# Optimization experiments

Measured on AMD Instinct MI355X. Metric: run time of the kernel, lower is better.

The kernel has to match this reference:

```python
import jax, jax.numpy as jnp
import numpy as np

K = 5  # kernel_size in context_loss
R = K // 2
COS_EPS = 1e-8  # F.cosine_similarity default eps


def _context_loss(er_input, seg_label, gt_boundary_seg):
    # er_input: [B,C,H,W] float; seg_label: [B,2,H,W] one-hot int; gt_boundary_seg: [B,H,W] int
    B, C, H, W = er_input.shape
    f32 = er_input.dtype

    gb = jnp.where(gt_boundary_seg == 255, 0, gt_boundary_seg)          # [B,H,W]
    slc = jnp.where(seg_label == 255, 0, seg_label)                     # [B,2,H,W]
    # gt_b = gt_boundary (broadcast over class dim) * seg_label; only channel 1 is used
    gt_b1 = gb * slc[:, 1]                                              # [B,H,W]
    boundary = gt_b1 > 0

    # interior margin so that all 5x5 neighbor shifts stay in-bounds
    iy = jnp.arange(H)
    ix = jnp.arange(W)
    interior = ((iy >= R) & (iy <= H - 1 - R))[:, None] & ((ix >= R) & (ix <= W - 1 - R))[None, :]
    sel = boundary & interior                                           # selected boundary pixels
    cnt = jnp.sum(sel, axis=(1, 2)).astype(f32)                         # [B]
    valid = jnp.sum(boundary, axis=(1, 2)) >= 1                         # batch participates (cal_mask.sum()>=1)

    nf = jnp.sqrt(jnp.sum(er_input * er_input, axis=1))                 # [B,H,W] feature norms
    seg_f = seg_label.astype(f32)

    shifts = [(ki - R, kj - R) for ki in range(K) for kj in range(K) if not (ki == R and kj == R)]
    loss_b = jnp.zeros((B,), f32)
    for dy, dx in shifts:
        # rolled[y,x] == orig[y+dy, x+dx]; wraparound is harmless since sel is interior-only
        fs = jnp.roll(er_input, (-dy, -dx), axis=(2, 3))
        ns = jnp.roll(nf, (-dy, -dx), axis=(1, 2))
        dot = jnp.sum(er_input * fs, axis=1)                            # [B,H,W]
        cos = dot / (jnp.maximum(nf, COS_EPS) * jnp.maximum(ns, COS_EPS))
        lab = jnp.sum(seg_f * jnp.roll(seg_f, (-dy, -dx), axis=(2, 3)), axis=1)
        se = jnp.where(sel, (cos - lab) ** 2, 0.0)
        loss_b = loss_b + jnp.sum(se, axis=(1, 2)) / jnp.maximum(cnt, 1.0)  # per-batch MSE for this shift
    loss_b = loss_b / len(shifts)

    n_valid = jnp.sum(valid.astype(f32))
    total = jnp.sum(jnp.where(valid, loss_b, 0.0)) / jnp.maximum(n_valid, 1.0)
    return jnp.where(jnp.isnan(total), jnp.zeros((), f32), total)


def setup_inputs() -> dict:
    key = jax.random.key(0)
    k1, k2, k3 = jax.random.split(key, 3)
    B, C, H, W = 4, 128, 384, 384
    er_input = jax.random.normal(k1, (B, C, H, W), dtype=jnp.float32)
    cls = jax.random.randint(k2, (B, H, W), 0, 2)
    seg_label = jnp.transpose(jax.nn.one_hot(cls, 2, dtype=jnp.int32), (0, 3, 1, 2))  # [B,2,H,W] one-hot
    gt_boundary_seg = jax.random.randint(k3, (B, H, W), 0, 2).astype(jnp.int32)
    return {"er_input": er_input, "seg_label": seg_label, "gt_boundary_seg": gt_boundary_seg}


def reference(er_input, seg_label, gt_boundary_seg):
    return _context_loss(er_input, seg_label, gt_boundary_seg)
```

## Files before the change

kernel.cpp:

```cpp
#include <hip/hip_runtime.h>
#include <math.h>

#define BB 4
#define CCH 128
#define HH 384
#define WW 384

constexpr int TILE_X = 64;
constexpr int TILE_Y = 16;
constexpr int CC = 4;
constexpr int NCHUNK = CCH / CC;
constexpr int ROWS = TILE_Y + 2;
constexpr int STR  = 72;
constexpr int GR   = 18;
constexpr int NVEC = CC * ROWS * GR;
constexpr int NLD  = 6;
constexpr int NSTR = 76;
#define EPSQ 1e-8f


__global__ __launch_bounds__(256, 3)
void ctx_main(const float* __restrict__ er, const int* __restrict__ seg,
              const int* __restrict__ gt, float* __restrict__ Ssum,
              int* __restrict__ cntArr, int* __restrict__ bndArr)
{
    __shared__ __align__(16) float buf0[CC * ROWS * STR];
    __shared__ __align__(16) float buf1[CC * ROWS * STR];
    __shared__ __align__(16) float normArr[ROWS * NSTR];

    const int tx  = threadIdx.x;
    const int ty  = threadIdx.y;
    const int tid = ty * 16 + tx;
    const int x0  = blockIdx.x * TILE_X;
    const int y0  = blockIdx.y * TILE_Y;
    const int b   = blockIdx.z;

    int srcOff[NLD];
    #pragma unroll
    for (int j = 0; j < NLD; ++j) {
        int id = tid + 256 * j; if (id > NVEC - 1) id = NVEC - 1;
        int c   = id / (ROWS * GR);
        int rem = id - c * (ROWS * GR);
        int r   = rem / GR;
        int g   = rem - r * GR;
        int gy  = y0 + r; if (gy > HH - 1) gy = HH - 1;
        int gx  = x0 - 4 + 4 * g;
        gx = min(max(gx, 0), WW - 4);
        srcOff[j] = (c * HH + gy) * WW + gx;
    }

    int hr = -1, hc = 0;
    if (tid < 136) { hr = TILE_Y + tid / 68; hc = 2 + tid % 68; }
    else if (tid < 200) {
        int t = tid - 136;
        hr = t >> 2;
        int j = t & 3;
        hc = (j < 2) ? (2 + j) : (66 + j);
    }

    float acc[12][4];
    #pragma unroll
    for (int s = 0; s < 12; ++s)
        #pragma unroll
        for (int i = 0; i < 4; ++i) acc[s][i] = 0.f;
    float nrm[4] = {0.f, 0.f, 0.f, 0.f};
    float haloN = 0.f;

    const float* erB = er + (size_t)b * CCH * HH * WW;

    auto issue = [&](int chunk, float* dst) {
        const float* erC = erB + (size_t)chunk * CC * HH * WW;
        #pragma unroll
        for (int j = 0; j < NLD; ++j) {
            int id = tid + 256 * j;
            if (j < NLD - 1 || id < NVEC) {
                __builtin_amdgcn_global_load_lds(
                    (const __attribute__((address_space(1))) void*)(erC + srcOff[j]),
                    (__attribute__((address_space(3))) void*)(dst + 4 * id),
                    16, 0, 0);
            }
        }
    };

    issue(0, buf0);

    for (int chunk = 0; chunk < NCHUNK; ++chunk) {
        float* cur = (chunk & 1) ? buf1 : buf0;
        __syncthreads();
        if (chunk + 1 < NCHUNK) issue(chunk + 1, (chunk & 1) ? buf0 : buf1);

        #pragma unroll
        for (int c = 0; c < CC; ++c) {
            const float* rp = &cur[(c * ROWS + ty) * STR + 4 * tx];
            float L0[12], L1[12], L2[12];
            #pragma unroll
            for (int jj = 0; jj < 3; ++jj) {
                *(float4*)&L0[4 * jj] = *(const float4*)(rp + 4 * jj);
                *(float4*)&L1[4 * jj] = *(const float4*)(rp + STR + 4 * jj);
                *(float4*)&L2[4 * jj] = *(const float4*)(rp + 2 * STR + 4 * jj);
            }
            #pragma unroll
            for (int i = 0; i < 4; ++i) {
                float f = L0[4 + i];
                nrm[i]    = fmaf(f, f,         nrm[i]);
                acc[0][i] = fmaf(f, L0[5 + i], acc[0][i]);
                acc[1][i] = fmaf(f, L0[6 + i], acc[1][i]);
                #pragma unroll
                for (int d = 0; d < 5; ++d) {
                    acc[2 + d][i] = fmaf(f, L1[2 + i + d], acc[2 + d][i]);
                    acc[7 + d][i] = fmaf(f, L2[2 + i + d], acc[7 + d][i]);
                }
            }
        }
        if (hr >= 0) {
            #pragma unroll
            for (int c = 0; c < CC; ++c) {
                float v = cur[(c * ROWS + hr) * STR + hc];
                haloN = fmaf(v, v, haloN);
            }
        }
    }

    __syncthreads();

    int* pkT = (int*)buf0;
    for (int it = tid; it < ROWS * STR; it += 256) {
        int r = it / STR, a = it - r * STR;
        int gy = y0 + r;
        int gx = x0 - 4 + a;
        int pk = 0;
        if (gy < HH && gx >= 0 && gx < WW) {
            int g   = gt[((size_t)b * HH + gy) * WW + gx];
            int gb  = (g == 255) ? 0 : g;
            int s0v = seg[(((size_t)b * 2 + 0) * HH + gy) * WW + gx];
            int s1v = seg[(((size_t)b * 2 + 1) * HH + gy) * WW + gx];
            int s1c = (s1v == 255) ? 0 : s1v;
            bool bnd   = (gb * s1c) > 0;
            bool inter = (gy >= 2 && gy <= HH - 3 && gx >= 2 && gx <= WW - 3);
            pk = (bnd ? 1 : 0) | ((bnd && inter) ? 2 : 0)
               | ((s0v & 255) << 8) | ((s1v & 255) << 16);
        }
        pkT[it] = pk;
    }
    #pragma unroll
    for (int i = 0; i < 4; ++i)
        normArr[ty * NSTR + 4 * tx + 4 + i] = sqrtf(nrm[i]);
    if (hr >= 0) normArr[hr * NSTR + hc] = sqrtf(haloN);
    __syncthreads();

    const float* nr = &normArr[ty * NSTR + 4 * tx];
    const int*   pr = &pkT[ty * STR + 4 * tx];
    float n0[12], n1[12], n2[12];
    int   p0[12], p1[12], p2[12];
    #pragma unroll
    for (int jj = 0; jj < 3; ++jj) {
        *(float4*)&n0[4 * jj] = *(const float4*)(nr + 4 * jj);
        *(float4*)&n1[4 * jj] = *(const float4*)(nr + NSTR + 4 * jj);
        *(float4*)&n2[4 * jj] = *(const float4*)(nr + 2 * NSTR + 4 * jj);
        *(int4*)&p0[4 * jj] = *(const int4*)(pr + 4 * jj);
        *(int4*)&p1[4 * jj] = *(const int4*)(pr + STR + 4 * jj);
        *(int4*)&p2[4 * jj] = *(const int4*)(pr + 2 * STR + 4 * jj);
    }

    float Sth = 0.f; int cth = 0, bth = 0;
    #pragma unroll
    for (int i = 0; i < 4; ++i) {
        int pkP  = p0[4 + i];
        int selP = (pkP >> 1) & 1;
        cth += selP;
        bth += pkP & 1;
        float nP = fmaxf(n0[4 + i], EPSQ);
        auto doPair = [&](float dot, int pkQ, float nQv) {
            int w = selP + ((pkQ >> 1) & 1);
            if (w) {
                float lab = (float)(((pkP >> 8) & 255) * ((pkQ >> 8) & 255)
                                  + ((pkP >> 16) & 255) * ((pkQ >> 16) & 255));
                float cs = dot / (nP * fmaxf(nQv, EPSQ));
                float d  = cs - lab;
                Sth = fmaf((float)w * d, d, Sth);
            }
        };
        doPair(acc[0][i], p0[5 + i], n0[5 + i]);
        doPair(acc[1][i], p0[6 + i], n0[6 + i]);
        #pragma unroll
        for (int d2 = 0; d2 < 5; ++d2) {
            doPair(acc[2 + d2][i], p1[2 + i + d2], n1[2 + i + d2]);
            doPair(acc[7 + d2][i], p2[2 + i + d2], n2[2 + i + d2]);
        }
    }

    #pragma unroll
    for (int off = 32; off > 0; off >>= 1) {
        Sth += __shfl_down(Sth, off);
        cth += __shfl_down(cth, off);
        bth += __shfl_down(bth, off);
    }
    if ((tid & 63) == 0) {
        atomicAdd(&Ssum[b], Sth);
        atomicAdd(&cntArr[b], cth);
        atomicAdd(&bndArr[b], bth);
    }
}

__global__ void ctx_init(float* S, int* cnt, int* bnd) {
    int t = threadIdx.x;
    if (t < BB) { S[t] = 0.f; cnt[t] = 0; bnd[t] = 0; }
}

__global__ void ctx_finalize(const float* __restrict__ S, const int* __restrict__ cnt,
                             const int* __restrict__ bnd, float* __restrict__ out) {
    if (threadIdx.x == 0 && blockIdx.x == 0) {
        float tot = 0.f, nv = 0.f;
        for (int b = 0; b < BB; ++b) {
            if (bnd[b] >= 1) {
                float c = fmaxf((float)cnt[b], 1.f);
                tot += S[b] / (24.f * c);
                nv  += 1.f;
            }
        }
        tot = tot / fmaxf(nv, 1.f);
        if (isnan(tot)) tot = 0.f;
        out[0] = tot;
    }
}

extern "C" void kernel_launch(void* const* d_in, const int* in_sizes, int n_in,
                              void* d_out, int out_size, void* d_ws, size_t ws_size,
                              hipStream_t stream) {
    const float* er = (const float*)d_in[0];
    const int* seg  = (const int*)d_in[1];
    const int* gt   = (const int*)d_in[2];
    float* out = (float*)d_out;

    float* S   = (float*)d_ws;
    int*   cnt = (int*)d_ws + BB;
    int*   bnd = (int*)d_ws + 2 * BB;

    ctx_init<<<1, 64, 0, stream>>>(S, cnt, bnd);
    dim3 grid(WW / TILE_X, HH / TILE_Y, BB);
    dim3 block(16, 16);
    ctx_main<<<grid, block, 0, stream>>>(er, seg, gt, S, cnt, bnd);
    ctx_finalize<<<1, 64, 0, stream>>>(S, cnt, bnd, out);
}
```

Measured before the change: 527.5 us.

## Load feature windows directly from global into registers, dropping LDS staging

Replaces the async global-to-LDS double-buffered channel staging with per-thread direct float4 global loads of a 3x12 window, software-pipelined across two register sets. The tile shrinks to 48x16 with 192 threads, and halo norms are gathered by edge and bottom-row threads. This removes the LDS traffic and per-chunk barriers but makes every thread reload overlapping neighbor data from global/L2 (about 2.25x redundant reads). It also raises register pressure and uses a less aligned block shape.

```diff
diff --git a/kernel.cpp b/kernel.cpp
--- a/kernel.cpp
+++ b/kernel.cpp
@@ -5,58 +5,49 @@
 #define CCH 128
 #define HH 384
 #define WW 384
-
-constexpr int TILE_X = 64;
-constexpr int TILE_Y = 16;
-constexpr int CC = 4;
-constexpr int NCHUNK = CCH / CC;
-constexpr int ROWS = TILE_Y + 2;
-constexpr int STR  = 72;
-constexpr int GR   = 18;
-constexpr int NVEC = CC * ROWS * GR;
-constexpr int NLD  = 6;
-constexpr int NSTR = 76;
+constexpr int HW = HH * WW;
+
+constexpr int TXG = 12;
+constexpr int TYR = 16;
+constexpr int PR   = 18;
+constexpr int NSTR = 56;
 #define EPSQ 1e-8f
 
 
-__global__ __launch_bounds__(256, 3)
+__global__ __launch_bounds__(192, 3)
 void ctx_main(const float* __restrict__ er, const int* __restrict__ seg,
               const int* __restrict__ gt, float* __restrict__ Ssum,
               int* __restrict__ cntArr, int* __restrict__ bndArr)
 {
-    __shared__ __align__(16) float buf0[CC * ROWS * STR];
-    __shared__ __align__(16) float buf1[CC * ROWS * STR];
-    __shared__ __align__(16) float normArr[ROWS * NSTR];
+    __shared__ int   pkT[PR * NSTR];
+    __shared__ float normArr[PR * NSTR];
 
     const int tx  = threadIdx.x;
     const int ty  = threadIdx.y;
-    const int tid = ty * 16 + tx;
-    const int x0  = blockIdx.x * TILE_X;
-    const int y0  = blockIdx.y * TILE_Y;
+    const int tid = ty * TXG + tx;
+    const int x0  = blockIdx.x * (4 * TXG);
+    const int y0  = blockIdx.y * TYR;
     const int b   = blockIdx.z;
 
-    int srcOff[NLD];
-    #pragma unroll
-    for (int j = 0; j < NLD; ++j) {
-        int id = tid + 256 * j; if (id > NVEC - 1) id = NVEC - 1;
-        int c   = id / (ROWS * GR);
-        int rem = id - c * (ROWS * GR);
-        int r   = rem / GR;
-        int g   = rem - r * GR;
-        int gy  = y0 + r; if (gy > HH - 1) gy = HH - 1;
-        int gx  = x0 - 4 + 4 * g;
-        gx = min(max(gx, 0), WW - 4);
-        srcOff[j] = (c * HH + gy) * WW + gx;
-    }
-
-    int hr = -1, hc = 0;
-    if (tid < 136) { hr = TILE_Y + tid / 68; hc = 2 + tid % 68; }
-    else if (tid < 200) {
-        int t = tid - 136;
-        hr = t >> 2;
-        int j = t & 3;
-        hc = (j < 2) ? (2 + j) : (66 + j);
-    }
+    const float* erB = er + (size_t)b * CCH * HW;
+
+    int off[3][3];
+    {
+        const int bcol = x0 + 4 * tx - 4;
+        #pragma unroll
+        for (int r = 0; r < 3; ++r) {
+            int gy = y0 + ty + r; if (gy > HH - 1) gy = HH - 1;
+            #pragma unroll
+            for (int j = 0; j < 3; ++j) {
+                int gc = bcol + 4 * j;
+                gc = min(max(gc, 0), WW - 4);
+                off[r][j] = gy * WW + gc;
+            }
+        }
+    }
+
+    const bool edge = (tx == 0) | (tx == TXG - 1);
+    const int  j0   = (tx == 0) ? 2 : 8;
 
     float acc[12][4];
     #pragma unroll
@@ -64,70 +55,74 @@
         #pragma unroll
         for (int i = 0; i < 4; ++i) acc[s][i] = 0.f;
     float nrm[4] = {0.f, 0.f, 0.f, 0.f};
-    float haloN = 0.f;
-
-    const float* erB = er + (size_t)b * CCH * HH * WW;
-
-    auto issue = [&](int chunk, float* dst) {
-        const float* erC = erB + (size_t)chunk * CC * HH * WW;
-        #pragma unroll
-        for (int j = 0; j < NLD; ++j) {
-            int id = tid + 256 * j;
-            if (j < NLD - 1 || id < NVEC) {
-                __builtin_amdgcn_global_load_lds(
-                    (const __attribute__((address_space(1))) void*)(erC + srcOff[j]),
-                    (__attribute__((address_space(3))) void*)(dst + 4 * id),
-                    16, 0, 0);
-            }
-        }
+    float ex[2]  = {0.f, 0.f};
+    float bh0[4] = {0.f, 0.f, 0.f, 0.f};
+    float bh1[4] = {0.f, 0.f, 0.f, 0.f};
+    float bhe[4] = {0.f, 0.f, 0.f, 0.f};
+
+    float XA[3][12], XB[3][12];
+
+    auto LOADW = [&](float (&X)[3][12], int ch) {
+        const float* p = erB + (size_t)ch * HW;
+        #pragma unroll
+        for (int r = 0; r < 3; ++r)
+            #pragma unroll
+            for (int j = 0; j < 3; ++j)
+                *(float4*)&X[r][4 * j] = *(const float4*)(p + off[r][j]);
     };
 
-    issue(0, buf0);
-
-    for (int chunk = 0; chunk < NCHUNK; ++chunk) {
-        float* cur = (chunk & 1) ? buf1 : buf0;
-        __syncthreads();
-        if (chunk + 1 < NCHUNK) issue(chunk + 1, (chunk & 1) ? buf0 : buf1);
-
-        #pragma unroll
-        for (int c = 0; c < CC; ++c) {
-            const float* rp = &cur[(c * ROWS + ty) * STR + 4 * tx];
-            float L0[12], L1[12], L2[12];
-            #pragma unroll
-            for (int jj = 0; jj < 3; ++jj) {
-                *(float4*)&L0[4 * jj] = *(const float4*)(rp + 4 * jj);
-                *(float4*)&L1[4 * jj] = *(const float4*)(rp + STR + 4 * jj);
-                *(float4*)&L2[4 * jj] = *(const float4*)(rp + 2 * STR + 4 * jj);
-            }
+    auto COMPW = [&](float (&X)[3][12]) {
+        #pragma unroll
+        for (int i = 0; i < 4; ++i) {
+            float f = X[0][4 + i];
+            nrm[i]    = fmaf(f, f,           nrm[i]);
+            acc[0][i] = fmaf(f, X[0][5 + i], acc[0][i]);
+            acc[1][i] = fmaf(f, X[0][6 + i], acc[1][i]);
+            #pragma unroll
+            for (int d = 0; d < 5; ++d) {
+                acc[2 + d][i] = fmaf(f, X[1][2 + i + d], acc[2 + d][i]);
+                acc[7 + d][i] = fmaf(f, X[2][2 + i + d], acc[7 + d][i]);
+            }
+        }
+        if (edge) {
+            float a = X[0][j0], c = X[0][j0 + 1];
+            ex[0] = fmaf(a, a, ex[0]);
+            ex[1] = fmaf(c, c, ex[1]);
+        }
+        if (ty == TYR - 1) {
             #pragma unroll
             for (int i = 0; i < 4; ++i) {
-                float f = L0[4 + i];
-                nrm[i]    = fmaf(f, f,         nrm[i]);
-                acc[0][i] = fmaf(f, L0[5 + i], acc[0][i]);
-                acc[1][i] = fmaf(f, L0[6 + i], acc[1][i]);
-                #pragma unroll
-                for (int d = 0; d < 5; ++d) {
-                    acc[2 + d][i] = fmaf(f, L1[2 + i + d], acc[2 + d][i]);
-                    acc[7 + d][i] = fmaf(f, L2[2 + i + d], acc[7 + d][i]);
-                }
-            }
-        }
-        if (hr >= 0) {
-            #pragma unroll
-            for (int c = 0; c < CC; ++c) {
-                float v = cur[(c * ROWS + hr) * STR + hc];
-                haloN = fmaf(v, v, haloN);
-            }
-        }
-    }
-
-    __syncthreads();
-
-    int* pkT = (int*)buf0;
-    for (int it = tid; it < ROWS * STR; it += 256) {
-        int r = it / STR, a = it - r * STR;
+                float a = X[1][4 + i], c = X[2][4 + i];
+                bh0[i] = fmaf(a, a, bh0[i]);
+                bh1[i] = fmaf(c, c, bh1[i]);
+            }
+            if (edge) {
+                float a = X[1][j0], c = X[1][j0 + 1];
+                float d = X[2][j0], e = X[2][j0 + 1];
+                bhe[0] = fmaf(a, a, bhe[0]);
+                bhe[1] = fmaf(c, c, bhe[1]);
+                bhe[2] = fmaf(d, d, bhe[2]);
+                bhe[3] = fmaf(e, e, bhe[3]);
+            }
+        }
+    };
+
+    LOADW(XA, 0);
+    #pragma unroll 1
+    for (int ch = 0; ch < CCH - 2; ch += 2) {
+        LOADW(XB, ch + 1);
+        COMPW(XA);
+        LOADW(XA, ch + 2);
+        COMPW(XB);
+    }
+    LOADW(XB, CCH - 1);
+    COMPW(XA);
+    COMPW(XB);
+
+    for (int it = tid; it < PR * NSTR; it += TXG * TYR) {
+        int r = it / NSTR, a = it - r * NSTR;
         int gy = y0 + r;
-        int gx = x0 - 4 + a;
+        int gx = x0 + a - 4;
         int pk = 0;
         if (gy < HH && gx >= 0 && gx < WW) {
             int g   = gt[((size_t)b * HH + gy) * WW + gx];
@@ -145,55 +140,75 @@
     #pragma unroll
     for (int i = 0; i < 4; ++i)
         normArr[ty * NSTR + 4 * tx + 4 + i] = sqrtf(nrm[i]);
-    if (hr >= 0) normArr[hr * NSTR + hc] = sqrtf(haloN);
+    if (edge) {
+        int c0 = (tx == 0) ? 2 : 52;
+        normArr[ty * NSTR + c0]     = sqrtf(ex[0]);
+        normArr[ty * NSTR + c0 + 1] = sqrtf(ex[1]);
+    }
+    if (ty == TYR - 1) {
+        #pragma unroll
+        for (int i = 0; i < 4; ++i) {
+            normArr[16 * NSTR + 4 * tx + 4 + i] = sqrtf(bh0[i]);
+            normArr[17 * NSTR + 4 * tx + 4 + i] = sqrtf(bh1[i]);
+        }
+        if (edge) {
+            int c0 = (tx == 0) ? 2 : 52;
+            normArr[16 * NSTR + c0]     = sqrtf(bhe[0]);
+            normArr[16 * NSTR + c0 + 1] = sqrtf(bhe[1]);
+            normArr[17 * NSTR + c0]     = sqrtf(bhe[2]);
+            normArr[17 * NSTR + c0 + 1] = sqrtf(bhe[3]);
+        }
+    }
     __syncthreads();
 
-    const float* nr = &normArr[ty * NSTR + 4 * tx];
-    const int*   pr = &pkT[ty * STR + 4 * tx];
-    float n0[12], n1[12], n2[12];
-    int   p0[12], p1[12], p2[12];
+    float Sth = 0.f; int cth = 0, bth = 0;
+    {
+        const float* nr = &normArr[ty * NSTR + 4 * tx];
+        const int*   pr = &pkT[ty * NSTR + 4 * tx];
+        float n0[12], n1[12], n2[12];
+        int   p0[12], p1[12], p2[12];
+        #pragma unroll
+        for (int jj = 0; jj < 3; ++jj) {
+            *(float4*)&n0[4 * jj] = *(const float4*)(nr + 4 * jj);
+            *(float4*)&n1[4 * jj] = *(const float4*)(nr + NSTR + 4 * jj);
+            *(float4*)&n2[4 * jj] = *(const float4*)(nr + 2 * NSTR + 4 * jj);
+            *(int4*)&p0[4 * jj] = *(const int4*)(pr + 4 * jj);
+            *(int4*)&p1[4 * jj] = *(const int4*)(pr + NSTR + 4 * jj);
+            *(int4*)&p2[4 * jj] = *(const int4*)(pr + 2 * NSTR + 4 * jj);
+        }
+
+        #pragma unroll
+        for (int i = 0; i < 4; ++i) {
+            int pkP  = p0[4 + i];
+            int selP = (pkP >> 1) & 1;
+            cth += selP;
+            bth += pkP & 1;
+            float nP = fmaxf(n0[4 + i], EPSQ);
+            auto doPair = [&](float dot, int pkQ, float nQv) {
+                int wgt = selP + ((pkQ >> 1) & 1);
+                if (wgt) {
+                    float lab = (float)(((pkP >> 8) & 255) * ((pkQ >> 8) & 255)
+                                      + ((pkP >> 16) & 255) * ((pkQ >> 16) & 255));
+                    float cs = dot / (nP * fmaxf(nQv, EPSQ));
+                    float d  = cs - lab;
+                    Sth = fmaf((float)wgt * d, d, Sth);
+                }
+            };
+            doPair(acc[0][i], p0[5 + i], n0[5 + i]);
+            doPair(acc[1][i], p0[6 + i], n0[6 + i]);
+            #pragma unroll
+            for (int d2 = 0; d2 < 5; ++d2) {
+                doPair(acc[2 + d2][i], p1[2 + i + d2], n1[2 + i + d2]);
+                doPair(acc[7 + d2][i], p2[2 + i + d2], n2[2 + i + d2]);
+            }
+        }
+    }
+
     #pragma unroll
-    for (int jj = 0; jj < 3; ++jj) {
-        *(float4*)&n0[4 * jj] = *(const float4*)(nr + 4 * jj);
-        *(float4*)&n1[4 * jj] = *(const float4*)(nr + NSTR + 4 * jj);
-        *(float4*)&n2[4 * jj] = *(const float4*)(nr + 2 * NSTR + 4 * jj);
-        *(int4*)&p0[4 * jj] = *(const int4*)(pr + 4 * jj);
-        *(int4*)&p1[4 * jj] = *(const int4*)(pr + STR + 4 * jj);
-        *(int4*)&p2[4 * jj] = *(const int4*)(pr + 2 * STR + 4 * jj);
-    }
-
-    float Sth = 0.f; int cth = 0, bth = 0;
-    #pragma unroll
-    for (int i = 0; i < 4; ++i) {
-        int pkP  = p0[4 + i];
-        int selP = (pkP >> 1) & 1;
-        cth += selP;
-        bth += pkP & 1;
-        float nP = fmaxf(n0[4 + i], EPSQ);
-        auto doPair = [&](float dot, int pkQ, float nQv) {
-            int w = selP + ((pkQ >> 1) & 1);
-            if (w) {
-                float lab = (float)(((pkP >> 8) & 255) * ((pkQ >> 8) & 255)
-                                  + ((pkP >> 16) & 255) * ((pkQ >> 16) & 255));
-                float cs = dot / (nP * fmaxf(nQv, EPSQ));
-                float d  = cs - lab;
-                Sth = fmaf((float)w * d, d, Sth);
-            }
-        };
-        doPair(acc[0][i], p0[5 + i], n0[5 + i]);
-        doPair(acc[1][i], p0[6 + i], n0[6 + i]);
-        #pragma unroll
-        for (int d2 = 0; d2 < 5; ++d2) {
-            doPair(acc[2 + d2][i], p1[2 + i + d2], n1[2 + i + d2]);
-            doPair(acc[7 + d2][i], p2[2 + i + d2], n2[2 + i + d2]);
-        }
-    }
-
-    #pragma unroll
-    for (int off = 32; off > 0; off >>= 1) {
-        Sth += __shfl_down(Sth, off);
-        cth += __shfl_down(cth, off);
-        bth += __shfl_down(bth, off);
+    for (int off2 = 32; off2 > 0; off2 >>= 1) {
+        Sth += __shfl_down(Sth, off2);
+        cth += __shfl_down(cth, off2);
+        bth += __shfl_down(bth, off2);
     }
     if ((tid & 63) == 0) {
         atomicAdd(&Ssum[b], Sth);
@@ -237,8 +252,8 @@
     int*   bnd = (int*)d_ws + 2 * BB;
 
     ctx_init<<<1, 64, 0, stream>>>(S, cnt, bnd);
-    dim3 grid(WW / TILE_X, HH / TILE_Y, BB);
-    dim3 block(16, 16);
+    dim3 grid(WW / 48, HH / TYR, BB);
+    dim3 block(TXG, TYR);
     ctx_main<<<grid, block, 0, stream>>>(er, seg, gt, S, cnt, bnd);
     ctx_finalize<<<1, 64, 0, stream>>>(S, cnt, bnd, out);
 }
```

Measured after the change: 667.4 us. +26.5%, slower.
